# Performance work log

Measured on AMD Instinct MI355X. Metric: run time of the kernel, lower is better.

The kernel has to match this reference:

```python
import jax, jax.numpy as jnp
import numpy as np


def _relative_position_index(S):
    # Faithful to the torch buffer construction, computed once with numpy (static).
    coords = np.stack(np.meshgrid(np.arange(S), np.arange(S), indexing='ij'))  # (2,S,S)
    coords = coords.reshape(2, -1)                                             # (2,N)
    rel = coords[:, :, None] - coords[:, None, :]                              # (2,N,N)
    rel = rel.transpose(1, 2, 0).astype(np.int64)                              # (N,N,2)
    rel[:, :, 0] += S - 1
    rel[:, :, 1] += S - 1
    rel[:, :, 0] *= 2 * S - 1
    idx = rel.sum(-1)
    idx = idx[::-1, ::-1].copy()  # flipud(fliplr(...))
    return idx                    # (N,N) int64 in [0, (2S-1)^2)


def setup_inputs() -> dict:
    key = jax.random.key(0)
    ks = jax.random.split(key, 6)
    B, S, C, NH = 8, 32, 512, 16
    x = jax.random.normal(ks[0], (B, S, S, C), dtype=jnp.float32)
    qkv_w = jax.random.normal(ks[1], (3 * C, C), dtype=jnp.float32) * 0.02
    qkv_b = jax.random.normal(ks[2], (3 * C,), dtype=jnp.float32) * 0.02
    rpb = jax.random.normal(ks[3], (NH, 2 * S - 1, 2 * S - 1), dtype=jnp.float32) * 0.02
    proj_w = jax.random.normal(ks[4], (C, C), dtype=jnp.float32) * 0.02
    proj_b = jax.random.normal(ks[5], (C,), dtype=jnp.float32) * 0.02
    return {"x": x, "qkv_w": qkv_w, "qkv_b": qkv_b, "rpb": rpb,
            "proj_w": proj_w, "proj_b": proj_b}


def reference(x, qkv_w, qkv_b, rpb, proj_w, proj_b):
    B, H, W, C = x.shape
    N = H * W
    num_heads = rpb.shape[0]
    head_dim = C // num_heads
    scale = head_dim ** (-0.5)
    S = H

    idx = _relative_position_index(S)  # static numpy (N,N)

    qkv = x.reshape(B, N, C) @ qkv_w.T + qkv_b            # (B,N,3C)
    qkv = qkv.reshape(B, N, 3, num_heads, head_dim)
    qkv = jnp.transpose(qkv, (2, 0, 3, 1, 4))             # (3,B,h,N,d)
    q, k, v = qkv[0], qkv[1], qkv[2]

    attn = jnp.einsum('bhnd,bhmd->bhnm', q * scale, k)    # (B,h,N,N)
    # gather relative position bias: (h,(2S-1)^2)[:, idx] -> (h,N,N)
    bias = rpb.reshape(num_heads, -1)[:, idx]
    attn = jax.nn.softmax(attn + bias[None], axis=-1)

    out = jnp.einsum('bhnm,bhmd->bhnd', attn, v)          # (B,h,N,d)
    out = jnp.transpose(out, (0, 2, 1, 3)).reshape(B, H, W, C)
    return out @ proj_w.T + proj_b
```

## Files before the change

### kernel.cpp

```cpp
#include <hip/hip_runtime.h>

typedef __bf16 bf16x8 __attribute__((ext_vector_type(8)));
typedef float f32x4 __attribute__((ext_vector_type(4)));
typedef unsigned int u32x2 __attribute__((ext_vector_type(2)));
typedef unsigned short u16;
typedef unsigned int u32;

__device__ __forceinline__ float bf2f(u16 v) {
    union { unsigned u; float f; } x; x.u = ((unsigned)v) << 16; return x.f;
}
__device__ __forceinline__ u16 f2bf(float f) {
    union { float f; unsigned u; } x; x.f = f;
    unsigned r = x.u + 0x7fffu + ((x.u >> 16) & 1u);
    return (u16)(r >> 16);
}

__device__ __forceinline__ bool probe_is_f32(const void* xp) {
    const unsigned* p = (const unsigned*)xp;
    int hits = 0;
#pragma unroll
    for (int i = 0; i < 32; i++) {
        const unsigned e = (p[i] >> 7) & 0xffu;
        hits += (e >= 0x90u) ? 1 : 0;
    }
    return hits > 3;
}

__device__ __forceinline__ float ld1(const void* p, size_t i, bool isf32) {
    return isf32 ? ((const float*)p)[i] : bf2f(((const u16*)p)[i]);
}

__device__ __forceinline__ void gl2lds16(const void* g, void* l) {
    __builtin_amdgcn_global_load_lds(
        (const __attribute__((address_space(1))) u32*)g,
        (__attribute__((address_space(3))) u32*)l, 16, 0, 0);
}

__global__ __launch_bounds__(256)
void convert_inputs(const void* __restrict__ x, const void* __restrict__ qw,
                    const void* __restrict__ qb, const void* __restrict__ pw,
                    const void* __restrict__ pb, const void* __restrict__ rp,
                    u16* __restrict__ xbf, u16* __restrict__ qwbf,
                    u16* __restrict__ qbbf, u16* __restrict__ pwbf,
                    u16* __restrict__ pbbf, float* __restrict__ rpl2e)
{
    const bool isf32 = probe_is_f32(x);
    const int gid = blockIdx.x * 256 + threadIdx.x;
    const int gsz = gridDim.x * 256;

    struct Seg { const void* s; u16* d; int n; };
    const Seg segs[5] = {{x, xbf, 4194304}, {qw, qwbf, 786432}, {pw, pwbf, 262144},
                         {qb, qbbf, 1536}, {pb, pbbf, 512}};
    for (int t = 0; t < 5; t++) {
        const int n4 = segs[t].n >> 2;
        if (isf32) {
            const f32x4* s = (const f32x4*)segs[t].s;
            for (int i = gid; i < n4; i += gsz) {
                f32x4 v = s[i];
                ushort4 o;
                o.x = f2bf(v[0]); o.y = f2bf(v[1]); o.z = f2bf(v[2]); o.w = f2bf(v[3]);
                *(ushort4*)(segs[t].d + i * 4) = o;
            }
        } else {
            const ushort4* s = (const ushort4*)segs[t].s;
            for (int i = gid; i < n4; i += gsz) *(ushort4*)(segs[t].d + i * 4) = s[i];
        }
    }
    for (int i = gid; i < 63504; i += gsz)
        rpl2e[i] = ld1(rp, i, isf32) * 1.4426950408889634f;
}

template<int MODE, int BM>
__global__ __launch_bounds__(256, MODE == 1 ? 3 : 4)
void gemm_bt(const u16* __restrict__ A, const u16* __restrict__ W,
             const u16* __restrict__ bias, void* __restrict__ out,
             u16* __restrict__ q_out, u16* __restrict__ k_out, u16* __restrict__ v_out,
             const void* __restrict__ probe, int Nout, int K)
{
    __shared__ __align__(16) u16 As[2][BM * 32];
    __shared__ __align__(16) u16 Ws[2][128 * 32];
    constexpr int RW = BM / 32;

    const int tid  = threadIdx.x;
    const int lane = tid & 63;
    const int wave = tid >> 6;
    const int quad = lane >> 4;
    const int l16  = lane & 15;
    const int m0 = blockIdx.y * BM;
    const int n0 = blockIdx.x * 128;
    const int wm = (wave >> 1) * (BM / 2);
    const int wn = (wave & 1) * 64;

    f32x4 acc[RW][4] = {};

    for (int k0 = 0; k0 < K; k0 += 64) {
        __syncthreads();
        for (int u = 0; u < 2; u++) {
            {
                const u16* g = A + (size_t)(m0 + wave * 16 + (lane >> 2)) * K
                                 + k0 + u * 32 + (lane & 3) * 8;
                u16* l = As[u] + wave * 16 * 32;
                for (int p = 0; p < BM / 64; p++) gl2lds16(g + (size_t)p * 64 * K, l + p * 64 * 32);
            }
            {
                const u16* g = W + (size_t)(n0 + wave * 16 + (lane >> 2)) * K
                                 + k0 + u * 32 + (lane & 3) * 8;
                u16* l = Ws[u] + wave * 16 * 32;
                for (int p = 0; p < 2; p++) gl2lds16(g + (size_t)p * 64 * K, l + p * 64 * 32);
            }
        }
        __syncthreads();

        for (int u = 0; u < 2; u++) {
            bf16x8 af[RW], wf[4];
            for (int i = 0; i < RW; i++)
                af[i] = *(const bf16x8*)(As[u] + (wm + i * 16 + l16) * 32 + quad * 8);
            for (int j = 0; j < 4; j++)
                wf[j] = *(const bf16x8*)(Ws[u] + (wn + j * 16 + l16) * 32 + quad * 8);
            for (int i = 0; i < RW; i++)
                for (int j = 0; j < 4; j++)
                    acc[i][j] = __builtin_amdgcn_mfma_f32_16x16x32_bf16(af[i], wf[j], acc[i][j], 0, 0, 0);
        }
    }

    if (MODE == 0) {
        const bool isf32 = probe_is_f32(probe);
        for (int j = 0; j < 4; j++) {
            const int col = n0 + wn + j * 16 + l16;
            const float bv = bf2f(bias[col]);
            for (int i = 0; i < RW; i++) {
                const int rbase = m0 + wm + i * 16 + quad * 4;
                for (int r = 0; r < 4; r++) {
                    const float val = acc[i][j][r] + bv;
                    if (isf32) ((float*)out)[(size_t)(rbase + r) * Nout + col] = val;
                    else       ((u16*)out)[(size_t)(rbase + r) * Nout + col]  = f2bf(val);
                }
            }
        }
    } else {
        const int which = m0 >> 9;
        float bv[RW][4];
        for (int i = 0; i < RW; i++) {
            const int row4 = m0 + wm + i * 16 + quad * 4;
            for (int r = 0; r < 4; r++) bv[i][r] = bf2f(bias[row4 + r]);
        }
        for (int j = 0; j < 4; j++) {
            const int tok = n0 + wn + j * 16 + l16;
            const int bi = tok >> 10, t = tok & 1023;
            for (int i = 0; i < RW; i++) {
                const int row4 = m0 + wm + i * 16 + quad * 4;
                const int h = (row4 >> 5) & 15;
                const int c = row4 & 31;
                if (which == 2) {
                    for (int r = 0; r < 4; r++)
                        v_out[((size_t)(bi * 16 + h) * 32 + c + r) * 1024 + t] =
                            f2bf(acc[i][j][r] + bv[i][r]);
                } else {
                    u16* dst = which ? k_out : q_out;
                    ushort4 pk;
                    pk.x = f2bf(acc[i][j][0] + bv[i][0]);
                    pk.y = f2bf(acc[i][j][1] + bv[i][1]);
                    pk.z = f2bf(acc[i][j][2] + bv[i][2]);
                    pk.w = f2bf(acc[i][j][3] + bv[i][3]);
                    *(ushort4*)(dst + ((size_t)(bi * 16 + h) * 1024 + t) * 32 + c) = pk;
                }
            }
        }
    }
}

__global__ __launch_bounds__(256, 4)
void attn(const u16* __restrict__ q, const u16* __restrict__ k,
          const u16* __restrict__ vt, const float* __restrict__ rpl2e,
          u16* __restrict__ o)
{
    __shared__ __align__(16) u16 Ks[2][64 * 40];
    __shared__ __align__(16) u16 Vt[2][32 * 72];
    __shared__ float biasT[63 * 37];

    const int tid  = threadIdx.x;
    const int lane = tid & 63;
    const int wave = tid >> 6;
    const int quad = lane >> 4;
    const int l16  = lane & 15;

    const int h  = blockIdx.x;
    const int qt = blockIdx.y;
    const int b  = blockIdx.z;
    const int n0 = qt * 128;
    const size_t base = ((size_t)(b * 16 + h)) * 32768;

    {
        const int row0 = 28 - 4 * qt;
        for (int idx = tid; idx < 2205; idx += 256) {
            const int rr = idx / 63, cc = idx % 63;
            biasT[cc * 37 + rr] =
                rpl2e[(size_t)h * 3969 + (size_t)(row0 + rr) * 63 + cc];
        }
    }
    uint4 kreg = *(const uint4*)(k + base + (size_t)(tid >> 2) * 32 + (tid & 3) * 8);
    uint4 vreg = *(const uint4*)(vt + base + (size_t)(tid >> 3) * 1024 + (tid & 7) * 8);
    *(uint4*)(Ks[0] + (tid >> 2) * 40 + (tid & 3) * 8) = kreg;
    *(uint4*)(Vt[0] + (tid >> 3) * 72 + (tid & 7) * 8) = vreg;

    bf16x8 qf[2];
    for (int g = 0; g < 2; g++) {
        union { uint4 u; bf16x8 f; } cv;
        cv.u = *(const uint4*)(q + base + (size_t)(n0 + g * 64 + wave * 16 + l16) * 32 + quad * 8);
        qf[g] = cv.f;
    }
    __syncthreads();

    bf16x8 ones;
    for (int i = 0; i < 8; i++) ones[i] = (__bf16)1.0f;

    f32x4 o_acc[2][3] = {};
    const int bn = (wave & 1) * 16 + l16;
    const int w2 = wave >> 1;
    const float SC = 0.25503485724582146f;

    const int cb = quad * 4 + 31 - bn;
    float X0[8], X1[8], Y0[8], Y1[8];
#pragma unroll
    for (int ci = 0; ci < 8; ci++) {
        const int c37 = (cb + (ci >> 2) * 16 + (ci & 3)) * 37;
        X0[ci] = biasT[c37 + (1 - w2)];
        X1[ci] = biasT[c37 + (2 - w2)];
        Y0[ci] = biasT[c37 + (3 - w2)];
        Y1[ci] = biasT[c37 + (4 - w2)];
    }

    for (int kt = 0; kt < 16; kt++) {
        const int cur = kt & 1;
        if (kt < 15) {
            const int mn = (kt + 1) * 64;
            kreg = *(const uint4*)(k + base + (size_t)(mn + (tid >> 2)) * 32 + (tid & 3) * 8);
            vreg = *(const uint4*)(vt + base + (size_t)(tid >> 3) * 1024 + mn + (tid & 7) * 8);
        }

        bf16x8 kf[4];
#pragma unroll
        for (int j = 0; j < 4; j++)
            kf[j] = *(const bf16x8*)(Ks[cur] + (j * 16 + l16) * 40 + quad * 8);
        bf16x8 vf[2][2];
#pragma unroll
        for (int kc = 0; kc < 2; kc++)
#pragma unroll
            for (int ct = 0; ct < 2; ct++)
                vf[kc][ct] = *(const bf16x8*)(Vt[cur] + (ct * 16 + l16) * 72 + kc * 32 + quad * 8);

#pragma unroll
        for (int g = 0; g < 2; g++) {
            f32x4 s4[4];
            const f32x4 zero = {};
#pragma unroll
            for (int j = 0; j < 4; j++)
                s4[j] = __builtin_amdgcn_mfma_f32_16x16x32_bf16(kf[j], qf[g], zero, 0, 0, 0);

            u32 Aw[4], Bw[4];
#pragma unroll
            for (int j = 0; j < 4; j++) {
                u16 pk[4];
#pragma unroll
                for (int r = 0; r < 4; r++) {
                    const int ci = (j & 1) * 4 + r;
                    const float bval = (j >> 1) ? (g ? X1[ci] : Y1[ci])
                                                : (g ? X0[ci] : Y0[ci]);
                    const float pv = __builtin_amdgcn_exp2f(s4[j][r] * SC + bval);
                    union { __bf16 b; u16 u; } cv; cv.b = (__bf16)pv;
                    pk[r] = cv.u;
                }
                Aw[j] = ((u32)pk[1] << 16) | pk[0];
                Bw[j] = ((u32)pk[3] << 16) | pk[2];
            }

#pragma unroll
            for (int kc = 0; kc < 2; kc++) {
                u32x2 ra = __builtin_amdgcn_permlane32_swap(Aw[2 * kc], Aw[2 * kc + 1], false, false);
                u32x2 wa = __builtin_amdgcn_permlane16_swap(ra.x, ra.y, false, false);
                u32x2 rb = __builtin_amdgcn_permlane32_swap(Bw[2 * kc], Bw[2 * kc + 1], false, false);
                u32x2 wb = __builtin_amdgcn_permlane16_swap(rb.x, rb.y, false, false);
                union { u32 w[4]; bf16x8 f; } pa;
                pa.w[0] = wa.x; pa.w[1] = wb.x; pa.w[2] = wa.y; pa.w[3] = wb.y;
#pragma unroll
                for (int ct = 0; ct < 2; ct++)
                    o_acc[g][ct] = __builtin_amdgcn_mfma_f32_16x16x32_bf16(pa.f, vf[kc][ct], o_acc[g][ct], 0, 0, 0);
                o_acc[g][2] = __builtin_amdgcn_mfma_f32_16x16x32_bf16(pa.f, ones, o_acc[g][2], 0, 0, 0);
            }
        }

        if (kt < 15) {
#pragma unroll
            for (int ci = 0; ci < 8; ci++) { X0[ci] = Y0[ci]; X1[ci] = Y1[ci]; }
            const int nr = 2 * kt - w2 + 5;
#pragma unroll
            for (int ci = 0; ci < 8; ci++) {
                const int c37 = (cb + (ci >> 2) * 16 + (ci & 3)) * 37;
                Y0[ci] = biasT[c37 + nr];
                Y1[ci] = biasT[c37 + nr + 1];
            }
            *(uint4*)(Ks[cur ^ 1] + (tid >> 2) * 40 + (tid & 3) * 8) = kreg;
            *(uint4*)(Vt[cur ^ 1] + (tid >> 3) * 72 + (tid & 7) * 8) = vreg;
        }
        __syncthreads();
    }

    for (int g = 0; g < 2; g++)
        for (int r = 0; r < 4; r++) {
            const float inv = __builtin_amdgcn_rcpf(o_acc[g][2][r]);
            const int n = n0 + g * 64 + wave * 16 + quad * 4 + r;
            u16* orow = o + ((size_t)b * 1024 + n) * 512 + h * 32;
            orow[l16]      = f2bf(o_acc[g][0][r] * inv);
            orow[16 + l16] = f2bf(o_acc[g][1][r] * inv);
        }
}

extern "C" void kernel_launch(void* const* d_in, const int* in_sizes, int n_in,
                              void* d_out, int out_size, void* d_ws, size_t ws_size,
                              hipStream_t stream) {
    const void* x      = d_in[0];
    const void* qkv_w  = d_in[1];
    const void* qkv_b  = d_in[2];
    const void* rpb    = d_in[3];
    const void* proj_w = d_in[4];
    const void* proj_b = d_in[5];

    u16* ws    = (u16*)d_ws;
    u16* kb    = ws;
    u16* vb    = ws + 4194304;
    u16* xbf   = ws + 8388608;
    u16* ao    = xbf;
    u16* qwbf  = ws + 12582912;
    u16* pwbf  = ws + 13369344;
    u16* qbbf  = ws + 13631488;
    u16* pbbf  = ws + 13633024;
    float* rpl2e = (float*)(ws + 13633536);
    u16* qb    = (u16*)d_out;

    convert_inputs<<<1024, 256, 0, stream>>>(x, qkv_w, qkv_b, proj_w, proj_b, rpb,
                                             xbf, qwbf, qbbf, pwbf, pbbf, rpl2e);

    dim3 g1(8192 / 128, 1536 / 128);
    gemm_bt<1, 128><<<g1, 256, 0, stream>>>(qwbf, xbf, qbbf, nullptr, qb, kb, vb, x, 8192, 512);

    dim3 g2(16, 8, 8);
    attn<<<g2, 256, 0, stream>>>(qb, kb, vb, rpl2e, ao);

    dim3 g3(512 / 128, 8192 / 64);
    gemm_bt<0, 64><<<g3, 256, 0, stream>>>(ao, pwbf, pbbf, d_out, nullptr, nullptr, nullptr, x, 512, 512);
}
```

Baseline: 148.9 us.

## Halve attention query tile, drop LDS bias table, read bias from global

Result: no change. 149.6 us (+0.5%).

```diff
diff --git a/kernel.cpp b/kernel.cpp
--- a/kernel.cpp
+++ b/kernel.cpp
@@ -169,14 +169,13 @@
     }
 }
 
-__global__ __launch_bounds__(256, 4)
+__global__ __launch_bounds__(256, 8)
 void attn(const u16* __restrict__ q, const u16* __restrict__ k,
           const u16* __restrict__ vt, const float* __restrict__ rpl2e,
           u16* __restrict__ o)
 {
     __shared__ __align__(16) u16 Ks[2][64 * 40];
     __shared__ __align__(16) u16 Vt[2][32 * 72];
-    __shared__ float biasT[63 * 37];
 
     const int tid  = threadIdx.x;
     const int lane = tid & 63;
@@ -184,51 +183,35 @@
     const int quad = lane >> 4;
     const int l16  = lane & 15;
 
-    const int h  = blockIdx.x;
-    const int qt = blockIdx.y;
-    const int b  = blockIdx.z;
-    const int n0 = qt * 128;
+    const int h   = blockIdx.x;
+    const int qtp = blockIdx.y;
+    const int b   = blockIdx.z;
+    const int n0  = qtp * 64;
     const size_t base = ((size_t)(b * 16 + h)) * 32768;
 
-    {
-        const int row0 = 28 - 4 * qt;
-        for (int idx = tid; idx < 2205; idx += 256) {
-            const int rr = idx / 63, cc = idx % 63;
-            biasT[cc * 37 + rr] =
-                rpl2e[(size_t)h * 3969 + (size_t)(row0 + rr) * 63 + cc];
-        }
-    }
     uint4 kreg = *(const uint4*)(k + base + (size_t)(tid >> 2) * 32 + (tid & 3) * 8);
     uint4 vreg = *(const uint4*)(vt + base + (size_t)(tid >> 3) * 1024 + (tid & 7) * 8);
     *(uint4*)(Ks[0] + (tid >> 2) * 40 + (tid & 3) * 8) = kreg;
     *(uint4*)(Vt[0] + (tid >> 3) * 72 + (tid & 7) * 8) = vreg;
 
-    bf16x8 qf[2];
-    for (int g = 0; g < 2; g++) {
+    bf16x8 qf;
+    {
         union { uint4 u; bf16x8 f; } cv;
-        cv.u = *(const uint4*)(q + base + (size_t)(n0 + g * 64 + wave * 16 + l16) * 32 + quad * 8);
-        qf[g] = cv.f;
+        cv.u = *(const uint4*)(q + base + (size_t)(n0 + wave * 16 + l16) * 32 + quad * 8);
+        qf = cv.f;
     }
     __syncthreads();
 
     bf16x8 ones;
     for (int i = 0; i < 8; i++) ones[i] = (__bf16)1.0f;
 
-    f32x4 o_acc[2][3] = {};
+    f32x4 o_acc[3] = {};
     const int bn = (wave & 1) * 16 + l16;
     const int w2 = wave >> 1;
     const float SC = 0.25503485724582146f;
-
     const int cb = quad * 4 + 31 - bn;
-    float X0[8], X1[8], Y0[8], Y1[8];
-#pragma unroll
-    for (int ci = 0; ci < 8; ci++) {
-        const int c37 = (cb + (ci >> 2) * 16 + (ci & 3)) * 37;
-        X0[ci] = biasT[c37 + (1 - w2)];
-        X1[ci] = biasT[c37 + (2 - w2)];
-        Y0[ci] = biasT[c37 + (3 - w2)];
-        Y1[ci] = biasT[c37 + (4 - w2)];
-    }
+    const float* bp = rpl2e + (size_t)h * 3969 + cb;
+    const int rowc = 31 - 2 * qtp - w2;
 
     for (int kt = 0; kt < 16; kt++) {
         const int cur = kt & 1;
@@ -238,81 +221,71 @@
             vreg = *(const uint4*)(vt + base + (size_t)(tid >> 3) * 1024 + mn + (tid & 7) * 8);
         }
 
+        const float* rbw = bp + (size_t)(2 * kt + rowc) * 63;
+        float X0[8], X1[8];
+#pragma unroll
+        for (int ci = 0; ci < 8; ci++) {
+            const int coff = (ci >> 2) * 16 + (ci & 3);
+            X0[ci] = rbw[coff];
+            X1[ci] = rbw[63 + coff];
+        }
+
         bf16x8 kf[4];
 #pragma unroll
         for (int j = 0; j < 4; j++)
             kf[j] = *(const bf16x8*)(Ks[cur] + (j * 16 + l16) * 40 + quad * 8);
-        bf16x8 vf[2][2];
-#pragma unroll
-        for (int kc = 0; kc < 2; kc++)
-#pragma unroll
-            for (int ct = 0; ct < 2; ct++)
-                vf[kc][ct] = *(const bf16x8*)(Vt[cur] + (ct * 16 + l16) * 72 + kc * 32 + quad * 8);
-
-#pragma unroll
-        for (int g = 0; g < 2; g++) {
-            f32x4 s4[4];
-            const f32x4 zero = {};
-#pragma unroll
-            for (int j = 0; j < 4; j++)
-                s4[j] = __builtin_amdgcn_mfma_f32_16x16x32_bf16(kf[j], qf[g], zero, 0, 0, 0);
-
-            u32 Aw[4], Bw[4];
-#pragma unroll
-            for (int j = 0; j < 4; j++) {
-                u16 pk[4];
-#pragma unroll
-                for (int r = 0; r < 4; r++) {
-                    const int ci = (j & 1) * 4 + r;
-                    const float bval = (j >> 1) ? (g ? X1[ci] : Y1[ci])
-                                                : (g ? X0[ci] : Y0[ci]);
-                    const float pv = __builtin_amdgcn_exp2f(s4[j][r] * SC + bval);
-                    union { __bf16 b; u16 u; } cv; cv.b = (__bf16)pv;
-                    pk[r] = cv.u;
-                }
-                Aw[j] = ((u32)pk[1] << 16) | pk[0];
-                Bw[j] = ((u32)pk[3] << 16) | pk[2];
-            }
-
-#pragma unroll
-            for (int kc = 0; kc < 2; kc++) {
-                u32x2 ra = __builtin_amdgcn_permlane32_swap(Aw[2 * kc], Aw[2 * kc + 1], false, false);
-                u32x2 wa = __builtin_amdgcn_permlane16_swap(ra.x, ra.y, false, false);
-                u32x2 rb = __builtin_amdgcn_permlane32_swap(Bw[2 * kc], Bw[2 * kc + 1], false, false);
-                u32x2 wb = __builtin_amdgcn_permlane16_swap(rb.x, rb.y, false, false);
-                union { u32 w[4]; bf16x8 f; } pa;
-                pa.w[0] = wa.x; pa.w[1] = wb.x; pa.w[2] = wa.y; pa.w[3] = wb.y;
-#pragma unroll
-                for (int ct = 0; ct < 2; ct++)
-                    o_acc[g][ct] = __builtin_amdgcn_mfma_f32_16x16x32_bf16(pa.f, vf[kc][ct], o_acc[g][ct], 0, 0, 0);
-                o_acc[g][2] = __builtin_amdgcn_mfma_f32_16x16x32_bf16(pa.f, ones, o_acc[g][2], 0, 0, 0);
-            }
+
+        f32x4 s4[4];
+        const f32x4 zero = {};
+#pragma unroll
+        for (int j = 0; j < 4; j++)
+            s4[j] = __builtin_amdgcn_mfma_f32_16x16x32_bf16(kf[j], qf, zero, 0, 0, 0);
+
+        u32 Aw[4], Bw[4];
+#pragma unroll
+        for (int j = 0; j < 4; j++) {
+            u16 pk[4];
+#pragma unroll
+            for (int r = 0; r < 4; r++) {
+                const int ci = (j & 1) * 4 + r;
+                const float bval = (j >> 1) ? X1[ci] : X0[ci];
+                const float pv = __builtin_amdgcn_exp2f(s4[j][r] * SC + bval);
+                union { __bf16 b; u16 u; } cv; cv.b = (__bf16)pv;
+                pk[r] = cv.u;
+            }
+            Aw[j] = ((u32)pk[1] << 16) | pk[0];
+            Bw[j] = ((u32)pk[3] << 16) | pk[2];
+        }
+
+#pragma unroll
+        for (int kc = 0; kc < 2; kc++) {
+            const bf16x8 vf0 = *(const bf16x8*)(Vt[cur] + l16 * 72 + kc * 32 + quad * 8);
+            const bf16x8 vf1 = *(const bf16x8*)(Vt[cur] + (16 + l16) * 72 + kc * 32 + quad * 8);
+            u32x2 ra = __builtin_amdgcn_permlane32_swap(Aw[2 * kc], Aw[2 * kc + 1], false, false);
+            u32x2 wa = __builtin_amdgcn_permlane16_swap(ra.x, ra.y, false, false);
+            u32x2 rb2 = __builtin_amdgcn_permlane32_swap(Bw[2 * kc], Bw[2 * kc + 1], false, false);
+            u32x2 wb = __builtin_amdgcn_permlane16_swap(rb2.x, rb2.y, false, false);
+            union { u32 w[4]; bf16x8 f; } pa;
+            pa.w[0] = wa.x; pa.w[1] = wb.x; pa.w[2] = wa.y; pa.w[3] = wb.y;
+            o_acc[0] = __builtin_amdgcn_mfma_f32_16x16x32_bf16(pa.f, vf0, o_acc[0], 0, 0, 0);
+            o_acc[1] = __builtin_amdgcn_mfma_f32_16x16x32_bf16(pa.f, vf1, o_acc[1], 0, 0, 0);
+            o_acc[2] = __builtin_amdgcn_mfma_f32_16x16x32_bf16(pa.f, ones, o_acc[2], 0, 0, 0);
         }
 
         if (kt < 15) {
-#pragma unroll
-            for (int ci = 0; ci < 8; ci++) { X0[ci] = Y0[ci]; X1[ci] = Y1[ci]; }
-            const int nr = 2 * kt - w2 + 5;
-#pragma unroll
-            for (int ci = 0; ci < 8; ci++) {
-                const int c37 = (cb + (ci >> 2) * 16 + (ci & 3)) * 37;
-                Y0[ci] = biasT[c37 + nr];
-                Y1[ci] = biasT[c37 + nr + 1];
-            }
             *(uint4*)(Ks[cur ^ 1] + (tid >> 2) * 40 + (tid & 3) * 8) = kreg;
             *(uint4*)(Vt[cur ^ 1] + (tid >> 3) * 72 + (tid & 7) * 8) = vreg;
         }
         __syncthreads();
     }
 
-    for (int g = 0; g < 2; g++)
-        for (int r = 0; r < 4; r++) {
-            const float inv = __builtin_amdgcn_rcpf(o_acc[g][2][r]);
-            const int n = n0 + g * 64 + wave * 16 + quad * 4 + r;
-            u16* orow = o + ((size_t)b * 1024 + n) * 512 + h * 32;
-            orow[l16]      = f2bf(o_acc[g][0][r] * inv);
-            orow[16 + l16] = f2bf(o_acc[g][1][r] * inv);
-        }
+    for (int r = 0; r < 4; r++) {
+        const float inv = __builtin_amdgcn_rcpf(o_acc[2][r]);
+        const int n = n0 + wave * 16 + quad * 4 + r;
+        u16* orow = o + ((size_t)b * 1024 + n) * 512 + h * 32;
+        orow[l16]      = f2bf(o_acc[0][r] * inv);
+        orow[16 + l16] = f2bf(o_acc[1][r] * inv);
+    }
 }
 
 extern "C" void kernel_launch(void* const* d_in, const int* in_sizes, int n_in,
@@ -343,7 +316,7 @@
     dim3 g1(8192 / 128, 1536 / 128);
     gemm_bt<1, 128><<<g1, 256, 0, stream>>>(qwbf, xbf, qbbf, nullptr, qb, kb, vb, x, 8192, 512);
 
-    dim3 g2(16, 8, 8);
+    dim3 g2(16, 16, 8);
     attn<<<g2, 256, 0, stream>>>(qb, kb, vb, rpl2e, ao);
 
     dim3 g3(512 / 128, 8192 / 64);
```
